# Optimization experiments

Measured on AMD Instinct MI355X. Metric: run time of the kernel, lower is better.

## Reference

```python
import jax, jax.numpy as jnp
import numpy as np

B, T, DIM, HEADS = 8, 2048, 1024, 16
HD = DIM // HEADS


def setup_inputs() -> dict:
    key = jax.random.key(0)
    ks = jax.random.split(key, 12)
    s = 0.02
    z = jnp.zeros((DIM,), jnp.float32)
    return {
        "x": jax.random.normal(ks[0], (B, T, DIM), jnp.float32),
        "Wq": jax.random.normal(ks[1], (DIM, DIM), jnp.float32) * s,
        "bq": z,
        "Wk": jax.random.normal(ks[2], (DIM, DIM), jnp.float32) * s,
        "bk": z,
        "Wv": jax.random.normal(ks[3], (DIM, DIM), jnp.float32) * s,
        "bv": z,
        "w_rwkv": jax.random.normal(ks[4], (HEADS, HD), jnp.float32) * 0.5,
        "u_rwkv": jax.random.normal(ks[5], (HEADS, HD), jnp.float32) * 0.5,
        "Wo": jax.random.normal(ks[6], (DIM, DIM), jnp.float32) * s,
        "bo": z,
    }


def reference(x, Wq, bq, Wk, bk, Wv, bv, w_rwkv, u_rwkv, Wo, bo):
    N, T_, _ = x.shape
    # queries are computed but never used in the original forward
    _ = x @ Wq + bq
    k = (x @ Wk + bk).reshape(N, T_, HEADS, HD)
    v = (x @ Wv + bv).reshape(N, T_, HEADS, HD)
    kt = jnp.moveaxis(k, 1, 0)  # [T, N, H, D]
    vt = jnp.moveaxis(v, 1, 0)  # [T, N, H, D]

    u = u_rwkv  # [H, D] broadcasts against [N, H, D]
    w = w_rwkv

    def step(carry, kv):
        pp, aa, bb = carry
        k_t, v_t = kv
        # output at step t (with bonus u)
        ww = u + k_t
        qq = jnp.maximum(ww, pp)
        e1 = jnp.exp(pp - qq)
        e2 = jnp.exp(ww - qq)
        o_t = (e1 * aa + e2 * v_t) / (e1 * bb + e2)
        # state update (with decay w)
        ww2 = pp - w
        qq2 = jnp.maximum(ww2, k_t)
        e1b = jnp.exp(ww2 - qq2)
        e2b = jnp.exp(k_t - qq2)
        aa2 = e1b * aa + e2b * v_t
        bb2 = e1b * bb + e2b
        return (qq2, aa2, bb2), o_t

    init = (kt[0], vt[0], jnp.ones_like(kt[0]))  # pp, aa, bb
    _, o_rest = jax.lax.scan(step, init, (kt[1:], vt[1:]))  # [T-1, N, H, D]
    O = jnp.concatenate([vt[:1], o_rest], axis=0)  # O[0] = v[0]
    O = jnp.moveaxis(O, 0, 1).reshape(N, T_, -1)  # [N, T, dim]
    return O @ Wo + bo
```

## Files before the change

### kernel.cpp

```cpp
#include <hip/hip_runtime.h>

#define DIMSZ 1024
#define NB 8
#define TSEQ 2048
#define MTOT (NB*TSEQ)
#define CCH 64
#define LCH (TSEQ/CCH)
#define NCHAN (NB*DIMSZ)

typedef __attribute__((ext_vector_type(8))) short short8v;
typedef __attribute__((ext_vector_type(4))) float f32x4;

__device__ __forceinline__ unsigned short f2bf(float f) {
  unsigned int u; __builtin_memcpy(&u, &f, 4);
  unsigned int r = u + 0x7FFF + ((u >> 16) & 1);
  return (unsigned short)(r >> 16);
}
__device__ __forceinline__ float bf2f(unsigned short us) {
  unsigned int v = ((unsigned int)us) << 16;
  float f; __builtin_memcpy(&f, &v, 4); return f;
}

__global__ __launch_bounds__(256) void cast_x_kernel(
    const float* __restrict__ in, unsigned short* __restrict__ out) {
  int i = blockIdx.x * 256 + threadIdx.x;
  float4 f = reinterpret_cast<const float4*>(in)[i];
  uint2 o;
  o.x = (unsigned)f2bf(f.x) | ((unsigned)f2bf(f.y) << 16);
  o.y = (unsigned)f2bf(f.z) | ((unsigned)f2bf(f.w) << 16);
  reinterpret_cast<uint2*>(out)[i] = o;
}

__global__ __launch_bounds__(256) void transpose_cast_kernel(
    const float* __restrict__ W, unsigned short* __restrict__ WT) {
  __shared__ float tile[32][33];
  int tx = threadIdx.x & 31, ty = threadIdx.x >> 5;
  int row0 = blockIdx.y * 32, col0 = blockIdx.x * 32;
  #pragma unroll
  for (int j = 0; j < 32; j += 8)
    tile[ty + j][tx] = W[(size_t)(row0 + ty + j) * DIMSZ + col0 + tx];
  __syncthreads();
  #pragma unroll
  for (int j = 0; j < 32; j += 8)
    WT[(size_t)(col0 + ty + j) * DIMSZ + row0 + tx] = f2bf(tile[tx][ty + j]);
}

#define BM 128
#define BN 128
#define BKK 64
#define LDT 72

template<int OUTBF>
__global__ __launch_bounds__(256) void gemm_bt_kernel(
    const unsigned short* __restrict__ A,
    const unsigned short* __restrict__ BT,
    void* __restrict__ Cv,
    const float* __restrict__ bias0,
    const float* __restrict__ bias1,
    int M, int N, int K, int Nsplit) {
  __shared__ __align__(16) unsigned short As[BM][LDT];
  __shared__ __align__(16) unsigned short Bs[BN][LDT];
  const int tid  = threadIdx.x;
  const int brow = blockIdx.x * BM;
  const int bcol = blockIdx.y * BN;
  const int wid  = tid >> 6;
  const int lane = tid & 63;
  const int wr = wid >> 1, wc = wid & 1;
  const int lrow = lane & 15;
  const int lko  = (lane >> 4) * 8;

  f32x4 acc[4][4];
  #pragma unroll
  for (int m = 0; m < 4; ++m)
    #pragma unroll
    for (int n = 0; n < 4; ++n)
      acc[m][n] = (f32x4){0.f, 0.f, 0.f, 0.f};

  for (int k0 = 0; k0 < K; k0 += BKK) {
    #pragma unroll
    for (int j = 0; j < 4; ++j) {
      int i = j * 256 + tid;
      int r = i >> 3, s = i & 7;
      *reinterpret_cast<short8v*>(&As[r][s * 8]) =
          *reinterpret_cast<const short8v*>(&A[(size_t)(brow + r) * K + k0 + s * 8]);
      *reinterpret_cast<short8v*>(&Bs[r][s * 8]) =
          *reinterpret_cast<const short8v*>(&BT[(size_t)(bcol + r) * K + k0 + s * 8]);
    }
    __syncthreads();
    #pragma unroll
    for (int kk = 0; kk < BKK; kk += 32) {
      short8v af[4], bf[4];
      #pragma unroll
      for (int m = 0; m < 4; ++m)
        af[m] = *reinterpret_cast<const short8v*>(&As[wr * 64 + m * 16 + lrow][kk + lko]);
      #pragma unroll
      for (int n = 0; n < 4; ++n)
        bf[n] = *reinterpret_cast<const short8v*>(&Bs[wc * 64 + n * 16 + lrow][kk + lko]);
      #pragma unroll
      for (int m = 0; m < 4; ++m)
        #pragma unroll
        for (int n = 0; n < 4; ++n)
          acc[m][n] = __builtin_amdgcn_mfma_f32_16x16x32_bf16(af[m], bf[n], acc[m][n], 0, 0, 0);
    }
    __syncthreads();
  }

  const int orow = brow + wr * 64;
  const int ocol = bcol + wc * 64;
  #pragma unroll
  for (int n = 0; n < 4; ++n) {
    int col = ocol + n * 16 + lrow;
    float b = (col < Nsplit) ? bias0[col] : bias1[col - Nsplit];
    #pragma unroll
    for (int m = 0; m < 4; ++m) {
      #pragma unroll
      for (int r = 0; r < 4; ++r) {
        int row = orow + m * 16 + (lane >> 4) * 4 + r;
        float val = acc[m][n][r] + b;
        if (OUTBF) {
          ((unsigned short*)Cv)[(size_t)row * N + col] = f2bf(val);
        } else {
          ((float*)Cv)[(size_t)row * N + col] = val;
        }
      }
    }
  }
}


__global__ __launch_bounds__(256) void wkv_chunk_state_kernel(
    const unsigned short* __restrict__ kv,
    const float* __restrict__ wdec,
    float* __restrict__ stP, float* __restrict__ stA, float* __restrict__ stB) {
  int idx = blockIdx.x * 256 + threadIdx.x;
  int c = idx & 1023;
  int n = (idx >> 10) & (NB - 1);
  int chunk = idx >> 13;
  float w = wdec[c];
  const unsigned short* base = kv + (size_t)(n * TSEQ + chunk * LCH) * 2048 + c;
  float p = -1e30f, a = 0.f, b = 0.f;
  #pragma unroll 8
  for (int j = 0; j < LCH; ++j) {
    float kt = bf2f(base[(size_t)j * 2048]);
    float vt = bf2f(base[(size_t)j * 2048 + 1024]);
    float ww2 = p - w;
    float qq2 = fmaxf(ww2, kt);
    float e1 = __expf(ww2 - qq2);
    float e2 = __expf(kt - qq2);
    a = e1 * a + e2 * vt;
    b = e1 * b + e2;
    p = qq2;
  }
  stP[idx] = p; stA[idx] = a; stB[idx] = b;
}

__global__ __launch_bounds__(256) void wkv_scan_kernel(
    const float* __restrict__ wdec,
    float* __restrict__ stP, float* __restrict__ stA, float* __restrict__ stB) {
  int idx = blockIdx.x * 256 + threadIdx.x;
  int c = idx & 1023;
  float decay = (float)LCH * wdec[c];
  float p = -1e30f, a = 0.f, b = 0.f;
  for (int i = 0; i < CCH; ++i) {
    int off = i * NCHAN + idx;
    float pc = stP[off], ac = stA[off], bc = stB[off];
    stP[off] = p; stA[off] = a; stB[off] = b;
    float pd = p - decay;
    float q = fmaxf(pd, pc);
    float e1 = __expf(pd - q);
    float e2 = __expf(pc - q);
    a = e1 * a + e2 * ac;
    b = e1 * b + e2 * bc;
    p = q;
  }
}

__global__ __launch_bounds__(256) void wkv_out_kernel(
    const unsigned short* __restrict__ kv,
    const float* __restrict__ wdec, const float* __restrict__ ubon,
    const float* __restrict__ stP, const float* __restrict__ stA,
    const float* __restrict__ stB,
    unsigned short* __restrict__ O) {
  int idx = blockIdx.x * 256 + threadIdx.x;
  int c = idx & 1023;
  int n = (idx >> 10) & (NB - 1);
  int chunk = idx >> 13;
  float w = wdec[c], u = ubon[c];
  const unsigned short* base = kv + (size_t)(n * TSEQ + chunk * LCH) * 2048 + c;
  unsigned short* ob = O + (size_t)(n * TSEQ + chunk * LCH) * DIMSZ + c;
  float p = stP[idx], a = stA[idx], b = stB[idx];
  #pragma unroll 4
  for (int j = 0; j < LCH; ++j) {
    float kt = bf2f(base[(size_t)j * 2048]);
    float vt = bf2f(base[(size_t)j * 2048 + 1024]);
    float ww = u + kt;
    float qq = fmaxf(ww, p);
    float e1 = __expf(p - qq);
    float e2 = __expf(ww - qq);
    float num = e1 * a + e2 * vt;
    float den = e1 * b + e2;
    ob[(size_t)j * DIMSZ] = f2bf(num * __builtin_amdgcn_rcpf(den));
    float ww2 = p - w;
    float qq2 = fmaxf(ww2, kt);
    float e1b = __expf(ww2 - qq2);
    float e2b = __expf(kt - qq2);
    a = e1b * a + e2b * vt;
    b = e1b * b + e2b;
    p = qq2;
  }
}

extern "C" void kernel_launch(void* const* d_in, const int* in_sizes, int n_in,
                              void* d_out, int out_size, void* d_ws, size_t ws_size,
                              hipStream_t stream) {
  const float* x  = (const float*)d_in[0];
  const float* Wk = (const float*)d_in[3];
  const float* bk = (const float*)d_in[4];
  const float* Wv = (const float*)d_in[5];
  const float* bv = (const float*)d_in[6];
  const float* wr = (const float*)d_in[7];
  const float* ur = (const float*)d_in[8];
  const float* Wo = (const float*)d_in[9];
  const float* bo = (const float*)d_in[10];
  float* out = (float*)d_out;

  char* ws = (char*)d_ws;
  unsigned short* xb   = (unsigned short*)(ws);
  unsigned short* WTkv = (unsigned short*)(ws + 33554432);
  unsigned short* WoT  = (unsigned short*)(ws + 37748736);
  unsigned short* kvb  = (unsigned short*)(ws + 39845888);

  float* stP = out;
  float* stA = out + CCH * NCHAN;
  float* stB = out + 2 * CCH * NCHAN;

  cast_x_kernel<<<dim3(16384), dim3(256), 0, stream>>>(x, xb);
  transpose_cast_kernel<<<dim3(32, 32), dim3(256), 0, stream>>>(Wk, WTkv);
  transpose_cast_kernel<<<dim3(32, 32), dim3(256), 0, stream>>>(Wv, WTkv + 1024 * 1024);
  transpose_cast_kernel<<<dim3(32, 32), dim3(256), 0, stream>>>(Wo, WoT);

  gemm_bt_kernel<1><<<dim3(128, 16), dim3(256), 0, stream>>>(
      xb, WTkv, (void*)kvb, bk, bv, MTOT, 2048, 1024, 1024);

  wkv_chunk_state_kernel<<<dim3(CCH * NCHAN / 256), dim3(256), 0, stream>>>(
      kvb, wr, stP, stA, stB);
  wkv_scan_kernel<<<dim3(NCHAN / 256), dim3(256), 0, stream>>>(wr, stP, stA, stB);
  wkv_out_kernel<<<dim3(CCH * NCHAN / 256), dim3(256), 0, stream>>>(
      kvb, wr, ur, stP, stA, stB, xb);

  gemm_bt_kernel<0><<<dim3(128, 8), dim3(256), 0, stream>>>(
      xb, WoT, (void*)out, bo, bo, MTOT, 1024, 1024, 1024);
}
```

Before: 204.6 us.

## Use direct global-to-LDS loads in GEMM and process two channels per WKV thread

The GEMM tile loads now use global_load_lds to copy 16 bytes per lane straight from global memory into shared memory, which bypasses registers. The shared tiles lose their padding because of this, so the MFMA fragment reads may hit more LDS bank conflicts. The WKV chunk-state and output kernels now handle two adjacent channels per thread, using 32-bit packed bf16 loads and stores and float2 state accesses. This halves the thread count and widens the memory transactions, in exchange for more registers per thread and less parallelism.

```diff
diff --git a/kernel.cpp b/kernel.cpp
--- a/kernel.cpp
+++ b/kernel.cpp
@@ -19,6 +19,12 @@
 __device__ __forceinline__ float bf2f(unsigned short us) {
   unsigned int v = ((unsigned int)us) << 16;
   float f; __builtin_memcpy(&f, &v, 4); return f;
+}
+
+__device__ __forceinline__ void gload16(const void* g, void* l) {
+  __builtin_amdgcn_global_load_lds(
+      (const __attribute__((address_space(1))) void*)g,
+      (__attribute__((address_space(3))) void*)l, 16, 0, 0);
 }
 
 __global__ __launch_bounds__(256) void cast_x_kernel(
@@ -48,7 +54,6 @@
 #define BM 128
 #define BN 128
 #define BKK 64
-#define LDT 72
 
 template<int OUTBF>
 __global__ __launch_bounds__(256) void gemm_bt_kernel(
@@ -58,8 +63,8 @@
     const float* __restrict__ bias0,
     const float* __restrict__ bias1,
     int M, int N, int K, int Nsplit) {
-  __shared__ __align__(16) unsigned short As[BM][LDT];
-  __shared__ __align__(16) unsigned short Bs[BN][LDT];
+  __shared__ __align__(16) unsigned short As[BM][BKK];
+  __shared__ __align__(16) unsigned short Bs[BN][BKK];
   const int tid  = threadIdx.x;
   const int brow = blockIdx.x * BM;
   const int bcol = blockIdx.y * BN;
@@ -68,6 +73,8 @@
   const int wr = wid >> 1, wc = wid & 1;
   const int lrow = lane & 15;
   const int lko  = (lane >> 4) * 8;
+  const int grow = lane >> 3;
+  const int gcol = (lane & 7) * 8;
 
   f32x4 acc[4][4];
   #pragma unroll
@@ -79,12 +86,9 @@
   for (int k0 = 0; k0 < K; k0 += BKK) {
     #pragma unroll
     for (int j = 0; j < 4; ++j) {
-      int i = j * 256 + tid;
-      int r = i >> 3, s = i & 7;
-      *reinterpret_cast<short8v*>(&As[r][s * 8]) =
-          *reinterpret_cast<const short8v*>(&A[(size_t)(brow + r) * K + k0 + s * 8]);
-      *reinterpret_cast<short8v*>(&Bs[r][s * 8]) =
-          *reinterpret_cast<const short8v*>(&BT[(size_t)(bcol + r) * K + k0 + s * 8]);
+      int r = wid * 32 + j * 8;
+      gload16(&A [(size_t)(brow + r + grow) * K + k0 + gcol], &As[r][0]);
+      gload16(&BT[(size_t)(bcol + r + grow) * K + k0 + gcol], &Bs[r][0]);
     }
     __syncthreads();
     #pragma unroll
@@ -128,30 +132,41 @@
 }
 
 
+__device__ __forceinline__ void wkv_step(float& p, float& a, float& b,
+                                         float kt, float vt, float w) {
+  float ww2 = p - w;
+  float qq2 = fmaxf(ww2, kt);
+  float e1 = __expf(ww2 - qq2);
+  float e2 = __expf(kt - qq2);
+  a = e1 * a + e2 * vt;
+  b = e1 * b + e2;
+  p = qq2;
+}
+
 __global__ __launch_bounds__(256) void wkv_chunk_state_kernel(
     const unsigned short* __restrict__ kv,
     const float* __restrict__ wdec,
     float* __restrict__ stP, float* __restrict__ stA, float* __restrict__ stB) {
   int idx = blockIdx.x * 256 + threadIdx.x;
-  int c = idx & 1023;
-  int n = (idx >> 10) & (NB - 1);
-  int chunk = idx >> 13;
-  float w = wdec[c];
+  int cp = idx & 511;
+  int n = (idx >> 9) & (NB - 1);
+  int chunk = idx >> 12;
+  int c = cp * 2;
+  float2 w2 = *reinterpret_cast<const float2*>(&wdec[c]);
   const unsigned short* base = kv + (size_t)(n * TSEQ + chunk * LCH) * 2048 + c;
-  float p = -1e30f, a = 0.f, b = 0.f;
+  float p0 = -1e30f, a0 = 0.f, b0 = 0.f;
+  float p1 = -1e30f, a1 = 0.f, b1 = 0.f;
   #pragma unroll 8
   for (int j = 0; j < LCH; ++j) {
-    float kt = bf2f(base[(size_t)j * 2048]);
-    float vt = bf2f(base[(size_t)j * 2048 + 1024]);
-    float ww2 = p - w;
-    float qq2 = fmaxf(ww2, kt);
-    float e1 = __expf(ww2 - qq2);
-    float e2 = __expf(kt - qq2);
-    a = e1 * a + e2 * vt;
-    b = e1 * b + e2;
-    p = qq2;
-  }
-  stP[idx] = p; stA[idx] = a; stB[idx] = b;
+    unsigned int kk = *reinterpret_cast<const unsigned int*>(&base[(size_t)j * 2048]);
+    unsigned int vv = *reinterpret_cast<const unsigned int*>(&base[(size_t)j * 2048 + 1024]);
+    wkv_step(p0, a0, b0, bf2f(kk & 0xffff), bf2f(vv & 0xffff), w2.x);
+    wkv_step(p1, a1, b1, bf2f(kk >> 16),    bf2f(vv >> 16),    w2.y);
+  }
+  int soff = chunk * NCHAN + n * 1024 + c;
+  *reinterpret_cast<float2*>(&stP[soff]) = make_float2(p0, p1);
+  *reinterpret_cast<float2*>(&stA[soff]) = make_float2(a0, a1);
+  *reinterpret_cast<float2*>(&stB[soff]) = make_float2(b0, b1);
 }
 
 __global__ __launch_bounds__(256) void wkv_scan_kernel(
@@ -182,31 +197,36 @@
     const float* __restrict__ stB,
     unsigned short* __restrict__ O) {
   int idx = blockIdx.x * 256 + threadIdx.x;
-  int c = idx & 1023;
-  int n = (idx >> 10) & (NB - 1);
-  int chunk = idx >> 13;
-  float w = wdec[c], u = ubon[c];
+  int cp = idx & 511;
+  int n = (idx >> 9) & (NB - 1);
+  int chunk = idx >> 12;
+  int c = cp * 2;
+  float2 w2 = *reinterpret_cast<const float2*>(&wdec[c]);
+  float2 u2 = *reinterpret_cast<const float2*>(&ubon[c]);
   const unsigned short* base = kv + (size_t)(n * TSEQ + chunk * LCH) * 2048 + c;
   unsigned short* ob = O + (size_t)(n * TSEQ + chunk * LCH) * DIMSZ + c;
-  float p = stP[idx], a = stA[idx], b = stB[idx];
+  int soff = chunk * NCHAN + n * 1024 + c;
+  float2 pP = *reinterpret_cast<const float2*>(&stP[soff]);
+  float2 pA = *reinterpret_cast<const float2*>(&stA[soff]);
+  float2 pB = *reinterpret_cast<const float2*>(&stB[soff]);
+  float p0 = pP.x, a0 = pA.x, b0 = pB.x;
+  float p1 = pP.y, a1 = pA.y, b1 = pB.y;
   #pragma unroll 4
   for (int j = 0; j < LCH; ++j) {
-    float kt = bf2f(base[(size_t)j * 2048]);
-    float vt = bf2f(base[(size_t)j * 2048 + 1024]);
-    float ww = u + kt;
-    float qq = fmaxf(ww, p);
-    float e1 = __expf(p - qq);
-    float e2 = __expf(ww - qq);
-    float num = e1 * a + e2 * vt;
-    float den = e1 * b + e2;
-    ob[(size_t)j * DIMSZ] = f2bf(num * __builtin_amdgcn_rcpf(den));
-    float ww2 = p - w;
-    float qq2 = fmaxf(ww2, kt);
-    float e1b = __expf(ww2 - qq2);
-    float e2b = __expf(kt - qq2);
-    a = e1b * a + e2b * vt;
-    b = e1b * b + e2b;
-    p = qq2;
+    unsigned int kk = *reinterpret_cast<const unsigned int*>(&base[(size_t)j * 2048]);
+    unsigned int vv = *reinterpret_cast<const unsigned int*>(&base[(size_t)j * 2048 + 1024]);
+    float k0 = bf2f(kk & 0xffff), k1 = bf2f(kk >> 16);
+    float v0 = bf2f(vv & 0xffff), v1 = bf2f(vv >> 16);
+    float ww0 = u2.x + k0, ww1 = u2.y + k1;
+    float qq0 = fmaxf(ww0, p0), qq1 = fmaxf(ww1, p1);
+    float e10 = __expf(p0 - qq0), e20 = __expf(ww0 - qq0);
+    float e11 = __expf(p1 - qq1), e21 = __expf(ww1 - qq1);
+    float o0 = (e10 * a0 + e20 * v0) * __builtin_amdgcn_rcpf(e10 * b0 + e20);
+    float o1 = (e11 * a1 + e21 * v1) * __builtin_amdgcn_rcpf(e11 * b1 + e21);
+    *reinterpret_cast<unsigned int*>(&ob[(size_t)j * DIMSZ]) =
+        (unsigned)f2bf(o0) | ((unsigned)f2bf(o1) << 16);
+    wkv_step(p0, a0, b0, k0, v0, w2.x);
+    wkv_step(p1, a1, b1, k1, v1, w2.y);
   }
 }
 
@@ -242,10 +262,10 @@
   gemm_bt_kernel<1><<<dim3(128, 16), dim3(256), 0, stream>>>(
       xb, WTkv, (void*)kvb, bk, bv, MTOT, 2048, 1024, 1024);
 
-  wkv_chunk_state_kernel<<<dim3(CCH * NCHAN / 256), dim3(256), 0, stream>>>(
+  wkv_chunk_state_kernel<<<dim3(CCH * NB * 512 / 256), dim3(256), 0, stream>>>(
       kvb, wr, stP, stA, stB);
   wkv_scan_kernel<<<dim3(NCHAN / 256), dim3(256), 0, stream>>>(wr, stP, stA, stB);
-  wkv_out_kernel<<<dim3(CCH * NCHAN / 256), dim3(256), 0, stream>>>(
+  wkv_out_kernel<<<dim3(CCH * NB * 512 / 256), dim3(256), 0, stream>>>(
       kvb, wr, ur, stP, stA, stB, xb);
 
   gemm_bt_kernel<0><<<dim3(128, 8), dim3(256), 0, stream>>>(
```

Result: slower. 228.9 us (+11.9%).
